# Optimization experiments

Measured on AMD Instinct MI355X. Metric: run time of the kernel, lower is better.

Reference implementation:

```python
import jax, jax.numpy as jnp
import numpy as np

B, S, D, H, E = 8, 4096, 1024, 2048, 8


def setup_inputs() -> dict:
    key = jax.random.key(0)
    ks = jax.random.split(key, 7)
    scale = 0.02
    return {
        "x": jax.random.normal(ks[0], (B, S, D), dtype=jnp.float32),
        "W1": jax.random.normal(ks[1], (E, D, H), dtype=jnp.float32) * scale,
        "b1": jnp.zeros((E, H), dtype=jnp.float32),
        "W2": jax.random.normal(ks[2], (E, H, D), dtype=jnp.float32) * scale,
        "b2": jnp.zeros((E, D), dtype=jnp.float32),
        "Wg": jax.random.normal(ks[3], (D, E), dtype=jnp.float32) * scale,
        "bg": jnp.zeros((E,), dtype=jnp.float32),
    }


def reference(x, W1, b1, W2, b2, Wg, bg):
    # Gating: softmax then top-1 (argmax) routing.
    logits = jnp.einsum("bsd,de->bse", x, Wg) + bg          # [B,S,E]
    probs = jax.nn.softmax(logits, axis=-1)                    # [B,S,E]
    top1 = jnp.argmax(probs, axis=-1)                          # [B,S] int

    out = jnp.zeros_like(x)
    # Fixed, small expert count: loop over experts (jit-friendly, no dynamic
    # shapes). coef zeros out tokens not routed to expert e, matching the
    # masked scatter in the original (unrouted positions stay 0 -> impossible
    # with top-1 over all experts, but semantics are identical).
    for e in range(E):
        coef = jnp.where(top1 == e, probs[..., e], 0.0)[..., None]  # [B,S,1]
        h = jax.nn.gelu(jnp.einsum("bsd,dh->bsh", x, W1[e]) + b1[e],
                        approximate=False)                      # exact GELU, torch default
        y = jnp.einsum("bsh,hd->bsd", h, W2[e]) + b2[e]
        out = out + coef * y
    return out
```

## Files before the change

### kernel.cpp

```cpp
#include <hip/hip_runtime.h>
#include <hip/hip_bf16.h>
#include <math.h>

#define NTOK 32768
#define DD   1024
#define HH   2048
#define EE   8

#define BM 256
#define BN 256
#define BK 64
#define MAXT2 144
#define NBLK 128

typedef __bf16 bf16x8 __attribute__((ext_vector_type(8)));
typedef __bf16 bf16x4 __attribute__((ext_vector_type(4)));
typedef float  f32x4  __attribute__((ext_vector_type(4)));

__device__ __forceinline__ void gload_lds16(const void* g, void* l) {
  __builtin_amdgcn_global_load_lds((__attribute__((address_space(1))) void*)(g),
                                   (__attribute__((address_space(3))) void*)(l),
                                   16, 0, 0);
}

__device__ __forceinline__ float fast_gelu(float v) {
  float az = fabsf(v) * 0.70710678118654752f;
  float t = 1.0f / (1.0f + 0.3275911f * az);
  float poly = t * (0.254829592f + t * (-0.284496736f +
               t * (1.421413741f + t * (-1.453152027f + t * 1.061405429f))));
  float erfa = 1.0f - poly * __expf(-az * az);
  float s = copysignf(erfa, v);
  return 0.5f * v * (1.0f + s);
}

__global__ __launch_bounds__(256) void k_gating(
    const float* __restrict__ x, const float* __restrict__ wg,
    const float* __restrict__ bg, int* __restrict__ eid,
    float* __restrict__ coef, __bf16* __restrict__ xbf)
{
  int lane = threadIdx.x & 63;
  int wave = threadIdx.x >> 6;
  int t0 = blockIdx.x * 8 + wave * 2;

  const float* xr0 = x + (size_t)t0 * DD;
  const float* xr1 = x + (size_t)(t0 + 1) * DD;
  double s0[8] = {}, s1[8] = {};
#pragma unroll
  for (int it = 0; it < 4; ++it) {
    int c0 = it * 256 + lane * 4;
    float4 xa = *(const float4*)(xr0 + c0);
    float4 xb = *(const float4*)(xr1 + c0);
    bf16x4 ca, cb;
#pragma unroll
    for (int j = 0; j < 4; ++j) { ca[j] = (__bf16)(&xa.x)[j]; cb[j] = (__bf16)(&xb.x)[j]; }
    *(bf16x4*)(xbf + (size_t)t0 * DD + c0) = ca;
    *(bf16x4*)(xbf + (size_t)(t0 + 1) * DD + c0) = cb;
    const float* w = wg + (size_t)c0 * EE;
#pragma unroll
    for (int j = 0; j < 4; ++j) {
      double fa = (double)(&xa.x)[j];
      double fb = (double)(&xb.x)[j];
#pragma unroll
      for (int e2 = 0; e2 < 8; ++e2) {
        double wv = (double)w[j * EE + e2];
        s0[e2] += fa * wv;
        s1[e2] += fb * wv;
      }
    }
  }

  int sel = lane & 1, sel2 = (lane >> 1) & 1, sel3 = (lane >> 2) & 1;
  int e = (lane & 1) * 4 + (lane & 2) + ((lane >> 2) & 1);
  double bge = (double)bg[e];

#pragma unroll
  for (int tk = 0; tk < 2; ++tk) {
    double* s = tk ? s1 : s0;
    double v4[4];
#pragma unroll
    for (int j = 0; j < 4; ++j) {
      double keep = sel ? s[4 + j] : s[j];
      double send = sel ? s[j] : s[4 + j];
      v4[j] = keep + __shfl_xor(send, 1, 64);
    }
    double v2[2];
#pragma unroll
    for (int j = 0; j < 2; ++j) {
      double keep = sel2 ? v4[2 + j] : v4[j];
      double send = sel2 ? v4[j] : v4[2 + j];
      v2[j] = keep + __shfl_xor(send, 2, 64);
    }
    double keep = sel3 ? v2[1] : v2[0];
    double send = sel3 ? v2[0] : v2[1];
    double tt = keep + __shfl_xor(send, 4, 64);
    tt += __shfl_xor(tt, 8, 64);
    tt += __shfl_xor(tt, 16, 64);
    tt += __shfl_xor(tt, 32, 64);
    double logit = tt + bge;
    double ml = logit; int me = e;
#pragma unroll
    for (int d2 = 1; d2 < 8; d2 <<= 1) {
      double ol = __shfl_xor(ml, d2, 64);
      int oe = __shfl_xor(me, d2, 64);
      if (ol > ml || (ol == ml && oe < me)) { ml = ol; me = oe; }
    }
    double se = exp(logit - ml);
#pragma unroll
    for (int d2 = 1; d2 < 8; d2 <<= 1) se += __shfl_xor(se, d2, 64);
    if (lane == 0) {
      eid[t0 + tk] = me;
      coef[t0 + tk] = (float)(1.0 / se);
    }
  }
}

__global__ __launch_bounds__(256) void k_hist(const int* __restrict__ eid,
                                              int* __restrict__ bhist) {
  __shared__ int h[EE];
  if (threadIdx.x < EE) h[threadIdx.x] = 0;
  __syncthreads();
  int t = blockIdx.x * 256 + threadIdx.x;
  atomicAdd(&h[eid[t]], 1);
  __syncthreads();
  if (threadIdx.x < EE) bhist[blockIdx.x * EE + threadIdx.x] = h[threadIdx.x];
}

__global__ void k_scan(const int* __restrict__ bhist, int* __restrict__ offs,
                       int* __restrict__ bbase, int2* __restrict__ tiles) {
  __shared__ int counts_s[EE];
  __shared__ int offs_s[EE + 1];
  int lane = threadIdx.x;
  if (lane < EE) {
    int sum = 0;
    for (int b = 0; b < NBLK; ++b) sum += bhist[b * EE + lane];
    counts_s[lane] = sum;
  }
  __syncthreads();
  if (lane == 0) {
    int a = 0;
    for (int e = 0; e < EE; ++e) { offs_s[e] = a; offs[e] = a; a += counts_s[e]; }
    offs_s[EE] = a; offs[EE] = a;
    int nt = 0;
    for (int e = 0; e < EE; ++e)
      for (int mt = 0; mt * BM < counts_s[e]; ++mt) tiles[nt++] = make_int2(e, mt);
    for (; nt < MAXT2; ++nt) tiles[nt] = make_int2(-1, 0);
  }
  __syncthreads();
  if (lane < EE) {
    int run = offs_s[lane];
    for (int b = 0; b < NBLK; ++b) {
      bbase[b * EE + lane] = run;
      run += bhist[b * EE + lane];
    }
  }
}

__global__ __launch_bounds__(256) void k_scatter(const int* __restrict__ eid,
                                                 const int* __restrict__ bbase,
                                                 int* __restrict__ idx) {
  __shared__ int cur[EE];
  if (threadIdx.x < EE) cur[threadIdx.x] = bbase[blockIdx.x * EE + threadIdx.x];
  __syncthreads();
  int t = blockIdx.x * 256 + threadIdx.x;
  int e = eid[t];
  int p = atomicAdd(&cur[e], 1);
  idx[p] = t;
}

__global__ __launch_bounds__(256) void k_transpose(
    const float* __restrict__ w, __bf16* __restrict__ wt, int R, int C)
{
  __shared__ float tile[32][33];
  int e = blockIdx.z;
  int c0 = blockIdx.x * 32, rb = blockIdx.y * 256;
  const float* we = w + (size_t)e * R * C;
  __bf16* wte = wt + (size_t)e * R * C;
  int tx = threadIdx.x & 31, ty = threadIdx.x >> 5;
  for (int s = 0; s < 8; ++s) {
    int r0 = rb + s * 32;
#pragma unroll
    for (int j = 0; j < 32; j += 8)
      tile[ty + j][tx] = we[(size_t)(r0 + ty + j) * C + (c0 + tx)];
    __syncthreads();
#pragma unroll
    for (int j = 0; j < 32; j += 8)
      wte[(size_t)(c0 + ty + j) * R + (r0 + tx)] = (__bf16)tile[tx][ty + j];
    __syncthreads();
  }
}


#define STAGE_A(u, kk, slot) do { \
    gload_lds16(aSrc0 + (u) * 128 + (kk) * 64, sA + (slot) * 16384 + tid * 16); \
    gload_lds16(aSrc1 + (u) * 128 + (kk) * 64, sA + (slot) * 16384 + 8192 + tid * 16); \
  } while (0)
#define STAGE_B(u, kk, slot) do { \
    gload_lds16(bSrc0 + (u) * 128 + (kk) * 64, sB + (slot) * 16384 + tid * 16); \
    gload_lds16(bSrc1 + (u) * 128 + (kk) * 64, sB + (slot) * 16384 + 8192 + tid * 16); \
  } while (0)
#define LDA4(slot, mq) do { \
    const char* _b = sA + (slot) * 16384 + (mq) * 4096 + aoff; \
    af[0] = *(const bf16x8*)(_b); \
    af[1] = *(const bf16x8*)(_b + 1024); \
    af[2] = *(const bf16x8*)(_b + 2048); \
    af[3] = *(const bf16x8*)(_b + 3072); \
  } while (0)
#define LDB4(slot) do { \
    const char* _b = sB + (slot) * 16384 + boff; \
    bfr[0] = *(const bf16x8*)(_b); \
    bfr[1] = *(const bf16x8*)(_b + 1024); \
    bfr[2] = *(const bf16x8*)(_b + 2048); \
    bfr[3] = *(const bf16x8*)(_b + 3072); \
  } while (0)
#define MM16(mq) do { \
    __builtin_amdgcn_s_setprio(1); \
    _Pragma("unroll") \
    for (int _m = 0; _m < 4; ++_m) \
      _Pragma("unroll") \
      for (int _n = 0; _n < 4; ++_n) \
        acc[(mq) * 4 + _m][_n] = __builtin_amdgcn_mfma_f32_16x16x32_bf16( \
            af[_m], bfr[_n], acc[(mq) * 4 + _m][_n], 0, 0, 0); \
    __builtin_amdgcn_s_setprio(0); \
  } while (0)
#define BAR_IN()  do { __builtin_amdgcn_s_barrier(); __builtin_amdgcn_sched_barrier(0); } while (0)
#define BAR_OUT() do { __builtin_amdgcn_s_barrier(); } while (0)
#define VM8()  asm volatile("s_waitcnt vmcnt(8)" ::: "memory")
#define VM4()  asm volatile("s_waitcnt vmcnt(4)" ::: "memory")
#define VM0()  asm volatile("s_waitcnt vmcnt(0)" ::: "memory")

template <int NT>
__device__ __forceinline__ void moe_mainloop(
    const char* aSrc0, const char* aSrc1, const char* bSrc0, const char* bSrc1,
    char* sA, char* sB, int tid, int aoff, int boff, f32x4 (&acc)[8][4])
{
  bf16x8 af[4], bfr[4];

  STAGE_A(0, 0, 0); STAGE_B(0, 0, 0);
  STAGE_A(0, 1, 1); STAGE_B(0, 1, 1);
  STAGE_A(1, 0, 2); STAGE_B(1, 0, 2);
  VM8();
  BAR_OUT();

  for (int t2 = 0; t2 < NT / 2 - 1; ++t2) {
    const int u1 = 2 * t2 + 1, u2 = 2 * t2 + 2, u3 = 2 * t2 + 3;
    LDA4(0, 0); LDB4(0);
    STAGE_A(u1, 1, 3);
    BAR_IN(); MM16(0); BAR_OUT();
    LDA4(0, 1);
    STAGE_B(u1, 1, 3);
    BAR_IN(); MM16(1); VM8(); BAR_OUT();
    LDA4(1, 0); LDB4(1);
    STAGE_A(u2, 0, 0);
    BAR_IN(); MM16(0); BAR_OUT();
    LDA4(1, 1);
    STAGE_B(u2, 0, 0);
    BAR_IN(); MM16(1); VM8(); BAR_OUT();
    LDA4(2, 0); LDB4(2);
    STAGE_A(u2, 1, 1);
    BAR_IN(); MM16(0); BAR_OUT();
    LDA4(2, 1);
    STAGE_B(u2, 1, 1);
    BAR_IN(); MM16(1); VM8(); BAR_OUT();
    LDA4(3, 0); LDB4(3);
    STAGE_A(u3, 0, 2);
    BAR_IN(); MM16(0); BAR_OUT();
    LDA4(3, 1);
    STAGE_B(u3, 0, 2);
    BAR_IN(); MM16(1); VM8(); BAR_OUT();
  }

  {
    const int u1 = NT - 1;
    LDA4(0, 0); LDB4(0);
    STAGE_A(u1, 1, 3);
    BAR_IN(); MM16(0); BAR_OUT();
    LDA4(0, 1);
    STAGE_B(u1, 1, 3);
    BAR_IN(); MM16(1); VM8(); BAR_OUT();
    LDA4(1, 0); LDB4(1);
    BAR_IN(); MM16(0); BAR_OUT();
    LDA4(1, 1);
    BAR_IN(); MM16(1); VM4(); BAR_OUT();
    LDA4(2, 0); LDB4(2);
    BAR_IN(); MM16(0); BAR_OUT();
    LDA4(2, 1);
    BAR_IN(); MM16(1); VM0(); BAR_OUT();
    LDA4(3, 0); LDB4(3);
    BAR_IN(); MM16(0); BAR_OUT();
    LDA4(3, 1);
    BAR_IN(); MM16(1);
  }
}

__global__ __launch_bounds__(512, 2) void k_gemm1(
    const __bf16* __restrict__ xbf, const __bf16* __restrict__ w1t,
    const float* __restrict__ b1, const int* __restrict__ idx,
    const int* __restrict__ offs, const int2* __restrict__ tiles,
    __bf16* __restrict__ hbuf)
{
  int2 te = tiles[blockIdx.x];
  int e = te.x;
  if (e < 0) return;
  int mt = te.y, nt = blockIdx.y;
  int off = offs[e], cnt = offs[e + 1] - off;
  int n0 = nt * BN;

  __shared__ __align__(16) char smem[131072];
  char* sA = smem;
  char* sB = smem + 65536;

  const int tid = threadIdx.x;
  const int lane = tid & 63;
  const int wid = tid >> 6;
  const int wr = wid >> 2, wc = wid & 3;
  const int lr = lane & 15, lk = lane >> 4;
  const int xorb = ((lr >> 3) & 1) << 1;
  const int aoff = (wr * 128 + lr) * 64 + ((lk ^ xorb) * 16);
  const int boff = (wc * 64 + lr) * 64 + ((lk ^ xorb) * 16);

  int row0 = tid >> 2, row1 = (512 + tid) >> 2;
  int g0 = (tid & 3) ^ (((row0 >> 3) & 1) << 1);
  int g1 = ((512 + tid) & 3) ^ (((row1 >> 3) & 1) << 1);
  int rl0 = mt * BM + row0; if (rl0 >= cnt) rl0 = cnt - 1;
  int rl1 = mt * BM + row1; if (rl1 >= cnt) rl1 = cnt - 1;
  const char* aSrc0 = (const char*)xbf + (size_t)idx[off + rl0] * (DD * 2) + g0 * 16;
  const char* aSrc1 = (const char*)xbf + (size_t)idx[off + rl1] * (DD * 2) + g1 * 16;
  const char* bSrc0 = (const char*)w1t + ((size_t)e * HH + n0 + row0) * (DD * 2) + g0 * 16;
  const char* bSrc1 = (const char*)w1t + ((size_t)e * HH + n0 + row1) * (DD * 2) + g1 * 16;

  f32x4 acc[8][4] = {};
  moe_mainloop<DD / BK>(aSrc0, aSrc1, bSrc0, bSrc1, sA, sB, tid, aoff, boff, acc);

#pragma unroll
  for (int m = 0; m < 8; ++m) {
    int rb = mt * BM + wr * 128 + m * 16 + lk * 4;
#pragma unroll
    for (int n = 0; n < 4; ++n) {
      int col = n0 + wc * 64 + n * 16 + lr;
      float bias = b1[e * HH + col];
#pragma unroll
      for (int j = 0; j < 4; ++j) {
        int r = rb + j;
        if (r < cnt)
          hbuf[(size_t)(off + r) * HH + col] = (__bf16)fast_gelu(acc[m][n][j] + bias);
      }
    }
  }
}

__global__ __launch_bounds__(512, 2) void k_gemm2(
    const __bf16* __restrict__ hbuf, const __bf16* __restrict__ w2t,
    const float* __restrict__ b2, const int* __restrict__ idx,
    const int* __restrict__ offs, const int2* __restrict__ tiles,
    const float* __restrict__ coef, float* __restrict__ out)
{
  int2 te = tiles[blockIdx.x];
  int e = te.x;
  if (e < 0) return;
  int mt = te.y, nt = blockIdx.y;
  int off = offs[e], cnt = offs[e + 1] - off;
  int n0 = nt * BN;

  __shared__ __align__(16) char smem[131072];
  char* sA = smem;
  char* sB = smem + 65536;

  const int tid = threadIdx.x;
  const int lane = tid & 63;
  const int wid = tid >> 6;
  const int wr = wid >> 2, wc = wid & 3;
  const int lr = lane & 15, lk = lane >> 4;
  const int xorb = ((lr >> 3) & 1) << 1;
  const int aoff = (wr * 128 + lr) * 64 + ((lk ^ xorb) * 16);
  const int boff = (wc * 64 + lr) * 64 + ((lk ^ xorb) * 16);

  int row0 = tid >> 2, row1 = (512 + tid) >> 2;
  int g0 = (tid & 3) ^ (((row0 >> 3) & 1) << 1);
  int g1 = ((512 + tid) & 3) ^ (((row1 >> 3) & 1) << 1);
  int rl0 = mt * BM + row0; if (rl0 >= cnt) rl0 = cnt - 1;
  int rl1 = mt * BM + row1; if (rl1 >= cnt) rl1 = cnt - 1;
  const char* aSrc0 = (const char*)hbuf + (size_t)(off + rl0) * (HH * 2) + g0 * 16;
  const char* aSrc1 = (const char*)hbuf + (size_t)(off + rl1) * (HH * 2) + g1 * 16;
  const char* bSrc0 = (const char*)w2t + ((size_t)e * DD + n0 + row0) * (HH * 2) + g0 * 16;
  const char* bSrc1 = (const char*)w2t + ((size_t)e * DD + n0 + row1) * (HH * 2) + g1 * 16;

  f32x4 acc[8][4] = {};
  moe_mainloop<HH / BK>(aSrc0, aSrc1, bSrc0, bSrc1, sA, sB, tid, aoff, boff, acc);

#pragma unroll
  for (int m = 0; m < 8; ++m) {
    int rb = mt * BM + wr * 128 + m * 16 + lk * 4;
#pragma unroll
    for (int j = 0; j < 4; ++j) {
      int r = rb + j;
      if (r < cnt) {
        int t = idx[off + r];
        float cf = coef[t];
#pragma unroll
        for (int n = 0; n < 4; ++n) {
          int col = n0 + wc * 64 + n * 16 + lr;
          out[(size_t)t * DD + col] = cf * (acc[m][n][j] + b2[e * DD + col]);
        }
      }
    }
  }
}

extern "C" void kernel_launch(void* const* d_in, const int* in_sizes, int n_in,
                              void* d_out, int out_size, void* d_ws, size_t ws_size,
                              hipStream_t stream)
{
  const float* x  = (const float*)d_in[0];
  const float* W1 = (const float*)d_in[1];
  const float* b1 = (const float*)d_in[2];
  const float* W2 = (const float*)d_in[3];
  const float* b2 = (const float*)d_in[4];
  const float* Wg = (const float*)d_in[5];
  const float* bg = (const float*)d_in[6];
  float* out = (float*)d_out;

  char* ws = (char*)d_ws;
  size_t o = 0;
  int* offs   = (int*)(ws + o); o += 64;
  int2* tiles = (int2*)(ws + o); o += MAXT2 * 8;
  int* bhist  = (int*)(ws + o); o += NBLK * EE * 4;
  int* bbase  = (int*)(ws + o); o += NBLK * EE * 4;
  int* eid    = (int*)(ws + o); o += (size_t)NTOK * 4;
  float* coef = (float*)(ws + o); o += (size_t)NTOK * 4;
  int* idx    = (int*)(ws + o); o += (size_t)NTOK * 4;
  o = (o + 255) & ~(size_t)255;
  __bf16* xbf = (__bf16*)(ws + o); o += (size_t)NTOK * DD * 2;
  __bf16* w1t = (__bf16*)(ws + o); o += (size_t)EE * HH * DD * 2;
  __bf16* w2t = (__bf16*)(ws + o); o += (size_t)EE * DD * HH * 2;
  __bf16* hbuf = (__bf16*)(ws + o); o += (size_t)NTOK * HH * 2;

  k_gating<<<NTOK / 8, 256, 0, stream>>>(x, Wg, bg, eid, coef, xbf);
  k_hist<<<NBLK, 256, 0, stream>>>(eid, bhist);
  k_scan<<<1, 64, 0, stream>>>(bhist, offs, bbase, tiles);
  k_scatter<<<NBLK, 256, 0, stream>>>(eid, bbase, idx);
  k_transpose<<<dim3(HH / 32, DD / 256, EE), 256, 0, stream>>>(W1, w1t, DD, HH);
  k_transpose<<<dim3(DD / 32, HH / 256, EE), 256, 0, stream>>>(W2, w2t, HH, DD);
  k_gemm1<<<dim3(MAXT2, HH / BN), 512, 0, stream>>>(xbf, w1t, b1, idx, offs, tiles, hbuf);
  k_gemm2<<<dim3(MAXT2, DD / BN), 512, 0, stream>>>(hbuf, w2t, b2, idx, offs, tiles, coef, out);
}
```

Baseline: 889.9 us.

## Rework MoE GEMM pipeline to BK=128 double buffer, grid swizzle, LDS-staged epilogues

New measurement: 862.6 us. 1.03x faster.

```diff
diff --git a/kernel.cpp b/kernel.cpp
--- a/kernel.cpp
+++ b/kernel.cpp
@@ -190,27 +190,31 @@
 }
 
 
-#define STAGE_A(u, kk, slot) do { \
-    gload_lds16(aSrc0 + (u) * 128 + (kk) * 64, sA + (slot) * 16384 + tid * 16); \
-    gload_lds16(aSrc1 + (u) * 128 + (kk) * 64, sA + (slot) * 16384 + 8192 + tid * 16); \
+#define STG(p, db, i, ko) \
+  gload_lds16((p) + (ko), (db) + (((i) * 512 + tid) * 16))
+#define STAGE_G1(nxt, ko) do { \
+    char* dA = sA + (nxt) * 32768; char* dB = sB + (nxt) * 32768; \
+    STG(aRB0, dA, 0, ko); STG(aRB2, dA, 2, ko); \
+    STG(bRB0, dB, 0, ko); STG(bRB1, dB, 1, ko); \
+    STG(bRB2, dB, 2, ko); STG(bRB3, dB, 3, ko); \
   } while (0)
-#define STAGE_B(u, kk, slot) do { \
-    gload_lds16(bSrc0 + (u) * 128 + (kk) * 64, sB + (slot) * 16384 + tid * 16); \
-    gload_lds16(bSrc1 + (u) * 128 + (kk) * 64, sB + (slot) * 16384 + 8192 + tid * 16); \
+#define STAGE_G2(nxt, ko) do { \
+    char* dA = sA + (nxt) * 32768; \
+    STG(aRB1, dA, 1, ko); STG(aRB3, dA, 3, ko); \
   } while (0)
-#define LDA4(slot, mq) do { \
-    const char* _b = sA + (slot) * 16384 + (mq) * 4096 + aoff; \
+#define LDA4(cur, mq, aoffk) do { \
+    const char* _b = sA + (cur) * 32768 + (mq) * 8192 + (aoffk); \
     af[0] = *(const bf16x8*)(_b); \
-    af[1] = *(const bf16x8*)(_b + 1024); \
-    af[2] = *(const bf16x8*)(_b + 2048); \
-    af[3] = *(const bf16x8*)(_b + 3072); \
+    af[1] = *(const bf16x8*)(_b + 2048); \
+    af[2] = *(const bf16x8*)(_b + 4096); \
+    af[3] = *(const bf16x8*)(_b + 6144); \
   } while (0)
-#define LDB4(slot) do { \
-    const char* _b = sB + (slot) * 16384 + boff; \
+#define LDB4(cur, boffk) do { \
+    const char* _b = sB + (cur) * 32768 + (boffk); \
     bfr[0] = *(const bf16x8*)(_b); \
-    bfr[1] = *(const bf16x8*)(_b + 1024); \
-    bfr[2] = *(const bf16x8*)(_b + 2048); \
-    bfr[3] = *(const bf16x8*)(_b + 3072); \
+    bfr[1] = *(const bf16x8*)(_b + 2048); \
+    bfr[2] = *(const bf16x8*)(_b + 4096); \
+    bfr[3] = *(const bf16x8*)(_b + 6144); \
   } while (0)
 #define MM16(mq) do { \
     __builtin_amdgcn_s_setprio(1); \
@@ -224,72 +228,48 @@
   } while (0)
 #define BAR_IN()  do { __builtin_amdgcn_s_barrier(); __builtin_amdgcn_sched_barrier(0); } while (0)
 #define BAR_OUT() do { __builtin_amdgcn_s_barrier(); } while (0)
-#define VM8()  asm volatile("s_waitcnt vmcnt(8)" ::: "memory")
-#define VM4()  asm volatile("s_waitcnt vmcnt(4)" ::: "memory")
+#define VM6()  asm volatile("s_waitcnt vmcnt(6)" ::: "memory")
+#define VM2()  asm volatile("s_waitcnt vmcnt(2)" ::: "memory")
 #define VM0()  asm volatile("s_waitcnt vmcnt(0)" ::: "memory")
 
 template <int NT>
 __device__ __forceinline__ void moe_mainloop(
-    const char* aSrc0, const char* aSrc1, const char* bSrc0, const char* bSrc1,
-    char* sA, char* sB, int tid, int aoff, int boff, f32x4 (&acc)[8][4])
+    const char* aRB0, const char* aRB1, const char* aRB2, const char* aRB3,
+    const char* bRB0, const char* bRB1, const char* bRB2, const char* bRB3,
+    char* sA, char* sB, int tid,
+    int aoff0, int aoff1, int boff0, int boff1, f32x4 (&acc)[8][4])
 {
   bf16x8 af[4], bfr[4];
 
-  STAGE_A(0, 0, 0); STAGE_B(0, 0, 0);
-  STAGE_A(0, 1, 1); STAGE_B(0, 1, 1);
-  STAGE_A(1, 0, 2); STAGE_B(1, 0, 2);
-  VM8();
+  STAGE_G1(0, 0);
+  STAGE_G2(0, 0);
+  VM2();
   BAR_OUT();
 
-  for (int t2 = 0; t2 < NT / 2 - 1; ++t2) {
-    const int u1 = 2 * t2 + 1, u2 = 2 * t2 + 2, u3 = 2 * t2 + 3;
-    LDA4(0, 0); LDB4(0);
-    STAGE_A(u1, 1, 3);
+  int cur = 0;
+  for (int u = 0; u < NT - 1; ++u) {
+    int nxt = cur ^ 1;
+    int ko = (u + 1) * 128;
+    STAGE_G1(nxt, ko);
+    LDA4(cur, 0, aoff0); LDB4(cur, boff0);
+    BAR_IN(); MM16(0); VM6(); BAR_OUT();
+    STAGE_G2(nxt, ko);
+    LDA4(cur, 1, aoff0);
+    BAR_IN(); MM16(1); BAR_OUT();
+    LDA4(cur, 0, aoff1); LDB4(cur, boff1);
     BAR_IN(); MM16(0); BAR_OUT();
-    LDA4(0, 1);
-    STAGE_B(u1, 1, 3);
-    BAR_IN(); MM16(1); VM8(); BAR_OUT();
-    LDA4(1, 0); LDB4(1);
-    STAGE_A(u2, 0, 0);
-    BAR_IN(); MM16(0); BAR_OUT();
-    LDA4(1, 1);
-    STAGE_B(u2, 0, 0);
-    BAR_IN(); MM16(1); VM8(); BAR_OUT();
-    LDA4(2, 0); LDB4(2);
-    STAGE_A(u2, 1, 1);
-    BAR_IN(); MM16(0); BAR_OUT();
-    LDA4(2, 1);
-    STAGE_B(u2, 1, 1);
-    BAR_IN(); MM16(1); VM8(); BAR_OUT();
-    LDA4(3, 0); LDB4(3);
-    STAGE_A(u3, 0, 2);
-    BAR_IN(); MM16(0); BAR_OUT();
-    LDA4(3, 1);
-    STAGE_B(u3, 0, 2);
-    BAR_IN(); MM16(1); VM8(); BAR_OUT();
-  }
-
-  {
-    const int u1 = NT - 1;
-    LDA4(0, 0); LDB4(0);
-    STAGE_A(u1, 1, 3);
-    BAR_IN(); MM16(0); BAR_OUT();
-    LDA4(0, 1);
-    STAGE_B(u1, 1, 3);
-    BAR_IN(); MM16(1); VM8(); BAR_OUT();
-    LDA4(1, 0); LDB4(1);
-    BAR_IN(); MM16(0); BAR_OUT();
-    LDA4(1, 1);
-    BAR_IN(); MM16(1); VM4(); BAR_OUT();
-    LDA4(2, 0); LDB4(2);
-    BAR_IN(); MM16(0); BAR_OUT();
-    LDA4(2, 1);
-    BAR_IN(); MM16(1); VM0(); BAR_OUT();
-    LDA4(3, 0); LDB4(3);
-    BAR_IN(); MM16(0); BAR_OUT();
-    LDA4(3, 1);
-    BAR_IN(); MM16(1);
-  }
+    LDA4(cur, 1, aoff1);
+    BAR_IN(); MM16(1); VM2(); BAR_OUT();
+    cur = nxt;
+  }
+  LDA4(cur, 0, aoff0); LDB4(cur, boff0);
+  BAR_IN(); MM16(0); VM0(); BAR_OUT();
+  LDA4(cur, 1, aoff0);
+  BAR_IN(); MM16(1); BAR_OUT();
+  LDA4(cur, 0, aoff1); LDB4(cur, boff1);
+  BAR_IN(); MM16(0); BAR_OUT();
+  LDA4(cur, 1, aoff1);
+  BAR_IN(); MM16(1);
 }
 
 __global__ __launch_bounds__(512, 2) void k_gemm1(
@@ -298,12 +278,17 @@
     const int* __restrict__ offs, const int2* __restrict__ tiles,
     __bf16* __restrict__ hbuf)
 {
-  int2 te = tiles[blockIdx.x];
+  int bid = blockIdx.x + 144 * blockIdx.y;
+  int bid2 = (bid & 7) * 144 + (bid >> 3);
+  int xt = bid2 % 144;
+  int yt = bid2 / 144;
+
+  int2 te = tiles[xt];
   int e = te.x;
   if (e < 0) return;
-  int mt = te.y, nt = blockIdx.y;
+  int mt = te.y;
   int off = offs[e], cnt = offs[e + 1] - off;
-  int n0 = nt * BN;
+  int n0 = yt * BN;
 
   __shared__ __align__(16) char smem[131072];
   char* sA = smem;
@@ -314,37 +299,56 @@
   const int wid = tid >> 6;
   const int wr = wid >> 2, wc = wid & 3;
   const int lr = lane & 15, lk = lane >> 4;
-  const int xorb = ((lr >> 3) & 1) << 1;
-  const int aoff = (wr * 128 + lr) * 64 + ((lk ^ xorb) * 16);
-  const int boff = (wc * 64 + lr) * 64 + ((lk ^ xorb) * 16);
-
-  int row0 = tid >> 2, row1 = (512 + tid) >> 2;
-  int g0 = (tid & 3) ^ (((row0 >> 3) & 1) << 1);
-  int g1 = ((512 + tid) & 3) ^ (((row1 >> 3) & 1) << 1);
-  int rl0 = mt * BM + row0; if (rl0 >= cnt) rl0 = cnt - 1;
-  int rl1 = mt * BM + row1; if (rl1 >= cnt) rl1 = cnt - 1;
-  const char* aSrc0 = (const char*)xbf + (size_t)idx[off + rl0] * (DD * 2) + g0 * 16;
-  const char* aSrc1 = (const char*)xbf + (size_t)idx[off + rl1] * (DD * 2) + g1 * 16;
-  const char* bSrc0 = (const char*)w1t + ((size_t)e * HH + n0 + row0) * (DD * 2) + g0 * 16;
-  const char* bSrc1 = (const char*)w1t + ((size_t)e * HH + n0 + row1) * (DD * 2) + g1 * 16;
+  const int ch0 = ((lk) ^ (lr & 7)) * 16;
+  const int ch1 = ((4 + lk) ^ (lr & 7)) * 16;
+  const int aoff0 = (wr * 128 + lr) * 128 + ch0;
+  const int aoff1 = (wr * 128 + lr) * 128 + ch1;
+  const int boff0 = (wc * 64 + lr) * 128 + ch0;
+  const int boff1 = (wc * 64 + lr) * 128 + ch1;
+
+  const int srow = tid >> 3;
+  const int chsw = ((tid & 7) ^ (srow & 7)) * 16;
+  const char* aRB[4];
+  const char* bRB[4];
+#pragma unroll
+  for (int i = 0; i < 4; ++i) {
+    int r = i * 64 + srow;
+    int rl = mt * BM + r; if (rl >= cnt) rl = cnt - 1;
+    aRB[i] = (const char*)xbf + (size_t)idx[off + rl] * (DD * 2) + chsw;
+    bRB[i] = (const char*)w1t + ((size_t)e * HH + n0 + r) * (DD * 2) + chsw;
+  }
 
   f32x4 acc[8][4] = {};
-  moe_mainloop<DD / BK>(aSrc0, aSrc1, bSrc0, bSrc1, sA, sB, tid, aoff, boff, acc);
-
-#pragma unroll
-  for (int m = 0; m < 8; ++m) {
-    int rb = mt * BM + wr * 128 + m * 16 + lk * 4;
-#pragma unroll
-    for (int n = 0; n < 4; ++n) {
-      int col = n0 + wc * 64 + n * 16 + lr;
-      float bias = b1[e * HH + col];
-#pragma unroll
-      for (int j = 0; j < 4; ++j) {
-        int r = rb + j;
-        if (r < cnt)
-          hbuf[(size_t)(off + r) * HH + col] = (__bf16)fast_gelu(acc[m][n][j] + bias);
-      }
-    }
+  moe_mainloop<DD / BK>(aRB[0], aRB[1], aRB[2], aRB[3],
+                        bRB[0], bRB[1], bRB[2], bRB[3],
+                        sA, sB, tid, aoff0, aoff1, boff0, boff1, acc);
+
+  __syncthreads();
+  char* wreg = smem + wid * 16384;
+  float bias[4];
+#pragma unroll
+  for (int n = 0; n < 4; ++n) bias[n] = b1[e * HH + n0 + wc * 64 + n * 16 + lr];
+#pragma unroll
+  for (int mq = 0; mq < 2; ++mq)
+#pragma unroll
+    for (int mm = 0; mm < 4; ++mm)
+#pragma unroll
+      for (int n = 0; n < 4; ++n)
+#pragma unroll
+        for (int j = 0; j < 4; ++j) {
+          int lrow = mq * 64 + mm * 16 + lk * 4 + j;
+          *(__bf16*)(wreg + (lrow * 64 + n * 16 + lr) * 2) =
+              (__bf16)fast_gelu(acc[mq * 4 + mm][n][j] + bias[n]);
+        }
+  asm volatile("s_waitcnt lgkmcnt(0)" ::: "memory");
+  int gcol = n0 + wc * 64 + (lane & 7) * 8;
+  int rowb = mt * BM + wr * 128 + (lane >> 3);
+#pragma unroll
+  for (int it = 0; it < 16; ++it) {
+    bf16x8 v = *(bf16x8*)(wreg + it * 1024 + lane * 16);
+    int grow = rowb + it * 8;
+    if (grow < cnt)
+      *(bf16x8*)((char*)hbuf + ((size_t)(off + grow) * HH + gcol) * 2) = v;
   }
 }
 
@@ -354,12 +358,17 @@
     const int* __restrict__ offs, const int2* __restrict__ tiles,
     const float* __restrict__ coef, float* __restrict__ out)
 {
-  int2 te = tiles[blockIdx.x];
+  int bid = blockIdx.x + 144 * blockIdx.y;
+  int bid2 = (bid & 7) * 72 + (bid >> 3);
+  int xt = bid2 % 144;
+  int yt = bid2 / 144;
+
+  int2 te = tiles[xt];
   int e = te.x;
   if (e < 0) return;
-  int mt = te.y, nt = blockIdx.y;
+  int mt = te.y;
   int off = offs[e], cnt = offs[e + 1] - off;
-  int n0 = nt * BN;
+  int n0 = yt * BN;
 
   __shared__ __align__(16) char smem[131072];
   char* sA = smem;
@@ -370,37 +379,60 @@
   const int wid = tid >> 6;
   const int wr = wid >> 2, wc = wid & 3;
   const int lr = lane & 15, lk = lane >> 4;
-  const int xorb = ((lr >> 3) & 1) << 1;
-  const int aoff = (wr * 128 + lr) * 64 + ((lk ^ xorb) * 16);
-  const int boff = (wc * 64 + lr) * 64 + ((lk ^ xorb) * 16);
-
-  int row0 = tid >> 2, row1 = (512 + tid) >> 2;
-  int g0 = (tid & 3) ^ (((row0 >> 3) & 1) << 1);
-  int g1 = ((512 + tid) & 3) ^ (((row1 >> 3) & 1) << 1);
-  int rl0 = mt * BM + row0; if (rl0 >= cnt) rl0 = cnt - 1;
-  int rl1 = mt * BM + row1; if (rl1 >= cnt) rl1 = cnt - 1;
-  const char* aSrc0 = (const char*)hbuf + (size_t)(off + rl0) * (HH * 2) + g0 * 16;
-  const char* aSrc1 = (const char*)hbuf + (size_t)(off + rl1) * (HH * 2) + g1 * 16;
-  const char* bSrc0 = (const char*)w2t + ((size_t)e * DD + n0 + row0) * (HH * 2) + g0 * 16;
-  const char* bSrc1 = (const char*)w2t + ((size_t)e * DD + n0 + row1) * (HH * 2) + g1 * 16;
+  const int ch0 = ((lk) ^ (lr & 7)) * 16;
+  const int ch1 = ((4 + lk) ^ (lr & 7)) * 16;
+  const int aoff0 = (wr * 128 + lr) * 128 + ch0;
+  const int aoff1 = (wr * 128 + lr) * 128 + ch1;
+  const int boff0 = (wc * 64 + lr) * 128 + ch0;
+  const int boff1 = (wc * 64 + lr) * 128 + ch1;
+
+  const int srow = tid >> 3;
+  const int chsw = ((tid & 7) ^ (srow & 7)) * 16;
+  const char* aRB[4];
+  const char* bRB[4];
+#pragma unroll
+  for (int i = 0; i < 4; ++i) {
+    int r = i * 64 + srow;
+    int rl = mt * BM + r; if (rl >= cnt) rl = cnt - 1;
+    aRB[i] = (const char*)hbuf + (size_t)(off + rl) * (HH * 2) + chsw;
+    bRB[i] = (const char*)w2t + ((size_t)e * DD + n0 + r) * (HH * 2) + chsw;
+  }
 
   f32x4 acc[8][4] = {};
-  moe_mainloop<HH / BK>(aSrc0, aSrc1, bSrc0, bSrc1, sA, sB, tid, aoff, boff, acc);
-
-#pragma unroll
-  for (int m = 0; m < 8; ++m) {
-    int rb = mt * BM + wr * 128 + m * 16 + lk * 4;
-#pragma unroll
-    for (int j = 0; j < 4; ++j) {
-      int r = rb + j;
-      if (r < cnt) {
-        int t = idx[off + r];
+  moe_mainloop<HH / BK>(aRB[0], aRB[1], aRB[2], aRB[3],
+                        bRB[0], bRB[1], bRB[2], bRB[3],
+                        sA, sB, tid, aoff0, aoff1, boff0, boff1, acc);
+
+  __syncthreads();
+  char* wreg = smem + wid * 16384;
+  float b2v[4];
+#pragma unroll
+  for (int n = 0; n < 4; ++n) b2v[n] = b2[e * DD + n0 + wc * 64 + n * 16 + lr];
+  int gcol = n0 + wc * 64 + (lane & 15) * 4;
+#pragma unroll
+  for (int pass = 0; pass < 2; ++pass) {
+    if (pass) asm volatile("s_waitcnt lgkmcnt(0)" ::: "memory");
+#pragma unroll
+    for (int mm = 0; mm < 4; ++mm)
+#pragma unroll
+      for (int n = 0; n < 4; ++n)
+#pragma unroll
+        for (int j = 0; j < 4; ++j) {
+          int lrow = mm * 16 + lk * 4 + j;
+          *(float*)(wreg + (lrow * 64 + n * 16 + lr) * 4) =
+              acc[pass * 4 + mm][n][j] + b2v[n];
+        }
+    asm volatile("s_waitcnt lgkmcnt(0)" ::: "memory");
+#pragma unroll
+    for (int it = 0; it < 16; ++it) {
+      float4 v = *(float4*)(wreg + it * 1024 + lane * 16);
+      int grow = mt * BM + wr * 128 + pass * 64 + it * 4 + (lane >> 4);
+      if (grow < cnt) {
+        int t = idx[off + grow];
         float cf = coef[t];
-#pragma unroll
-        for (int n = 0; n < 4; ++n) {
-          int col = n0 + wc * 64 + n * 16 + lr;
-          out[(size_t)t * DD + col] = cf * (acc[m][n][j] + b2[e * DD + col]);
-        }
+        float4 o;
+        o.x = v.x * cf; o.y = v.y * cf; o.z = v.z * cf; o.w = v.w * cf;
+        *(float4*)(out + (size_t)t * DD + gcol) = o;
       }
     }
   }
```
